# Performance work log

Measured on AMD Instinct MI355X. Metric: run time of the kernel, lower is better.

Reference implementation:

```python
import jax, jax.numpy as jnp
import numpy as np

B, T, C, H, W = 32, 64, 2, 32, 32
NK, KS = 16, 6          # n_kernels, kernel_size
ACT = 27                # conv output spatial size (32-6+1)
FEAT = ACT * ACT * NK   # 11664 flattened features
RU = 16                 # rnn_units
AD_RATE_L, REC_RATE_L = 0.1, 0.1   # AdaptiveLayer rates
AD_RATE_R, REC_RATE_R = 0.4, 0.1   # SimpleRNN rates


def setup_inputs() -> dict:
    key = jax.random.key(0)
    ks = jax.random.split(key, 8)
    stdv = 1.0 / np.sqrt(RU)
    return {
        "x": jax.random.normal(ks[0], (B, T, C, H, W), jnp.float32),
        "conv_w": jax.random.normal(ks[1], (NK, C, KS, KS), jnp.float32) * 0.01,
        "conv_b": jnp.full((NK,), 0.01, jnp.float32),
        "w_ih": jax.random.uniform(ks[2], (RU, FEAT), jnp.float32, -stdv, stdv),
        "w_hh": jax.random.uniform(ks[3], (RU, RU), jnp.float32, -stdv, stdv),
        "b_ih": jax.random.uniform(ks[4], (RU,), jnp.float32, -stdv, stdv),
        "b_hh": jax.random.uniform(ks[5], (RU,), jnp.float32, -stdv, stdv),
        "fc_w": jax.random.normal(ks[6], (2, RU), jnp.float32) * 0.01,
        "fc_b": jnp.full((2,), 0.01, jnp.float32),
    }


def reference(x, conv_w, conv_b, w_ih, w_hh, b_ih, b_hh, fc_w, fc_b):
    Bn, Tn = x.shape[:2]
    # per-frame conv: fold frames into batch
    xf = x.reshape(Bn * Tn, C, H, W)
    conv = jax.lax.conv_general_dilated(
        xf, conv_w, window_strides=(1, 1), padding='VALID',
        dimension_numbers=('NCHW', 'OIHW', 'NCHW'))
    conv = conv + conv_b[None, :, None, None]
    out_conv = conv.reshape(Bn, Tn, NK, ACT, ACT)
    out_flat = jax.nn.relu(out_conv.reshape(Bn, Tn, FEAT))

    # AdaptiveLayer: per-frame clamp/decay scan (initial adaptation is zeros)
    def ad_step(adapt, frame):
        out = jnp.maximum(frame - adapt, 0.0)
        adapt = (adapt + AD_RATE_L * out) * (1.0 - REC_RATE_L)
        return adapt, out
    _, adapted = jax.lax.scan(ad_step, jnp.zeros((Bn, FEAT), x.dtype),
                              jnp.swapaxes(out_flat, 0, 1))
    out_adapted = jnp.swapaxes(adapted, 0, 1)  # [B,T,FEAT]

    # SimpleRNN with adaptation state
    def rnn_step(carry, x_t):
        h, adapt = carry
        pre = x_t @ w_ih.T + b_ih + h @ w_hh.T + b_hh
        a = jnp.maximum(pre - adapt, 0.0)
        adapt = (adapt + AD_RATE_R * a) * (1.0 - REC_RATE_R)
        h = jax.nn.relu(a)
        return (h, adapt), h
    h0 = jnp.zeros((Bn, RU), x.dtype)
    _, hs = jax.lax.scan(rnn_step, (h0, h0), jnp.swapaxes(out_adapted, 0, 1))
    out_rnn = jnp.swapaxes(hs, 0, 1)  # [B,T,RU]

    out_fc = out_rnn @ fc_w.T + fc_b  # [B,T,2]
    return (out_fc, out_conv, out_flat, out_rnn)
```

## Files before the change

kernel.cpp:

```cpp
#include <hip/hip_runtime.h>

#define FEAT 11664
#define OFF_FC   0u
#define OFF_CONV 4096u
#define OFF_FLAT 23891968u
#define OFF_RNN  47779840u

static __device__ __forceinline__ unsigned short f2bf(float f) {
    unsigned int u = __float_as_uint(f);
    u += 0x7FFFu + ((u >> 16) & 1u);
    return (unsigned short)(u >> 16);
}

__global__ __launch_bounds__(128) void k_conv(const float* __restrict__ x,
                                              const float* __restrict__ cw,
                                              const float* __restrict__ cb,
                                              float* __restrict__ out)
{
    __shared__ __align__(16) float smem[11664];
    __shared__ float bls[16];
    float* xs  = smem;
    float* wls = smem + 2304;
    float* ot  = smem;
    const int tid = threadIdx.x;
    const int frame = blockIdx.x;

    const float4* xg = (const float4*)(x + (size_t)frame * 2048);
    for (int c0 = tid; c0 < 512; c0 += 128) {
        float4 v = xg[c0];
        int e0 = c0 * 4;
        int ch = e0 >> 10, rem = e0 & 1023, row = rem >> 5, col = rem & 31;
        float* dst = &xs[ch * 1152 + row * 36 + col];
        dst[0] = v.x; dst[1] = v.y; dst[2] = v.z; dst[3] = v.w;
    }
    for (int idx = tid; idx < 1152; idx += 128) {
        int k = idx / 72;
        int rem = idx - k * 72;
        wls[rem * 16 + k] = cw[idx];
    }
    if (tid < 16) bls[tid] = cb[tid];
    __syncthreads();

    const int kg = tid >> 5;
    const int r  = tid & 31;
    float acc[4][27];
    if (r < 27) {
        #pragma unroll
        for (int kk = 0; kk < 4; ++kk)
            #pragma unroll
            for (int c = 0; c < 27; ++c) acc[kk][c] = 0.f;

        for (int ch = 0; ch < 2; ++ch) {
            for (int i = 0; i < 6; ++i) {
                const float* rowp = &xs[ch * 1152 + (r + i) * 36];
                float xr[32];
                #pragma unroll
                for (int m = 0; m < 8; ++m) {
                    float4 v = ((const float4*)rowp)[m];
                    xr[4*m+0] = v.x; xr[4*m+1] = v.y; xr[4*m+2] = v.z; xr[4*m+3] = v.w;
                }
                float4 wj[6];
                #pragma unroll
                for (int j = 0; j < 6; ++j)
                    wj[j] = *(const float4*)&wls[(ch * 36 + i * 6 + j) * 16 + kg * 4];
                #pragma unroll
                for (int j = 0; j < 6; ++j) {
                    #pragma unroll
                    for (int c = 0; c < 27; ++c) {
                        float xv = xr[c + j];
                        acc[0][c] = fmaf(xv, wj[j].x, acc[0][c]);
                        acc[1][c] = fmaf(xv, wj[j].y, acc[1][c]);
                        acc[2][c] = fmaf(xv, wj[j].z, acc[2][c]);
                        acc[3][c] = fmaf(xv, wj[j].w, acc[3][c]);
                    }
                }
            }
        }
    }

    __syncthreads();
    if (r < 27) {
        #pragma unroll
        for (int kk = 0; kk < 4; ++kk) {
            float bv = bls[kg * 4 + kk];
            float* dst = &ot[(kg * 4 + kk) * 729 + r * 27];
            #pragma unroll
            for (int c = 0; c < 27; ++c) dst[c] = acc[kk][c] + bv;
        }
    }
    __syncthreads();

    const float4* src4 = (const float4*)ot;
    float4* dc = (float4*)(out + OFF_CONV + (size_t)frame * FEAT);
    float4* df = (float4*)(out + OFF_FLAT + (size_t)frame * FEAT);
    for (int e = tid; e < 2916; e += 128) {
        float4 v = src4[e];
        dc[e] = v;
        float4 rv;
        rv.x = v.x > 0.f ? v.x : 0.f;
        rv.y = v.y > 0.f ? v.y : 0.f;
        rv.z = v.z > 0.f ? v.z : 0.f;
        rv.w = v.w > 0.f ? v.w : 0.f;
        df[e] = rv;
    }
}

typedef short bf16x8 __attribute__((ext_vector_type(8)));
typedef float f32x4  __attribute__((ext_vector_type(4)));

__global__ __launch_bounds__(256) void k_adapt_proj(const float* __restrict__ flat,
                                                    const float* __restrict__ w_ih,
                                                    float* __restrict__ partial)
{
    __shared__ __align__(16) unsigned short A[16 * 744];
    __shared__ __align__(16) unsigned short Bw[16 * 744];
    __shared__ __align__(16) float accscr[4 * 64 * 4];
    const int tid = threadIdx.x;
    const int b  = blockIdx.x >> 4;
    const int fb = blockIdx.x & 15;
    const int fbase = fb * 729;

    float v0[16], v1[16], v2[16];
    const float* src0 = flat + (size_t)(b * 64) * FEAT + fbase + tid * 3;
    if (tid < 243) {
        #pragma unroll
        for (int tl = 0; tl < 16; ++tl) {
            const float* p = src0 + (size_t)tl * FEAT;
            v0[tl] = p[0]; v1[tl] = p[1]; v2[tl] = p[2];
        }
    }

    for (int n = 0; n < 16; ++n) {
        const float* src = w_ih + (size_t)n * FEAT + fbase;
        for (int f = tid; f < 729; f += 256) Bw[n * 744 + f] = f2bf(src[f]);
    }
    if (tid < 240) {
        int n = tid / 15, c = 729 + (tid % 15);
        A[n * 744 + c]  = 0;
        Bw[n * 744 + c] = 0;
    }
    __syncthreads();

    float ad0 = 0.f, ad1 = 0.f, ad2 = 0.f;
    const int w = tid >> 6, l = tid & 63;
    const int m = l & 15, q = l >> 4;

    for (int tt = 0; tt < 4; ++tt) {
        if (tid < 243) {
            unsigned short* arow = &A[tid * 3];
            #pragma unroll
            for (int tl = 0; tl < 16; ++tl) {
                float o0 = fmaxf(v0[tl] - ad0, 0.f); ad0 = (ad0 + 0.1f * o0) * 0.9f;
                float o1 = fmaxf(v1[tl] - ad1, 0.f); ad1 = (ad1 + 0.1f * o1) * 0.9f;
                float o2 = fmaxf(v2[tl] - ad2, 0.f); ad2 = (ad2 + 0.1f * o2) * 0.9f;
                unsigned short* dst = arow + tl * 744;
                dst[0] = f2bf(o0); dst[1] = f2bf(o1); dst[2] = f2bf(o2);
            }
        }
        __syncthreads();

        if (tt < 3 && tid < 243) {
            const float* srcn = flat + (size_t)(b * 64 + (tt + 1) * 16) * FEAT + fbase + tid * 3;
            #pragma unroll
            for (int tl = 0; tl < 16; ++tl) {
                const float* p = srcn + (size_t)tl * FEAT;
                v0[tl] = p[0]; v1[tl] = p[1]; v2[tl] = p[2];
            }
        }

        f32x4 acc = {0.f, 0.f, 0.f, 0.f};
        for (int s = w; s < 23; s += 4) {
            int k0 = s * 32;
            bf16x8 av = *(const bf16x8*)&A [m * 744 + k0 + q * 8];
            bf16x8 bv = *(const bf16x8*)&Bw[m * 744 + k0 + q * 8];
            acc = __builtin_amdgcn_mfma_f32_16x16x32_bf16(av, bv, acc, 0, 0, 0);
        }
        *(f32x4*)&accscr[(w * 64 + l) * 4] = acc;
        __syncthreads();
        {
            int ll = tid >> 2, rg = tid & 3;
            float s = accscr[(0 * 64 + ll) * 4 + rg] + accscr[(1 * 64 + ll) * 4 + rg]
                    + accscr[(2 * 64 + ll) * 4 + rg] + accscr[(3 * 64 + ll) * 4 + rg];
            int row = ((ll >> 4) * 4) + rg;
            int col = ll & 15;
            partial[(size_t)(((fb * 32 + b) * 64 + tt * 16 + row) * 16) + col] = s;
        }
        __syncthreads();
    }
}

__global__ __launch_bounds__(64) void k_rnn(const float* __restrict__ partial,
                                            const float* __restrict__ w_hh,
                                            const float* __restrict__ b_ih,
                                            const float* __restrict__ b_hh,
                                            const float* __restrict__ fc_w,
                                            const float* __restrict__ fc_b,
                                            float* __restrict__ out)
{
    __shared__ __align__(16) float preL[4096];
    __shared__ float hL[64];
    const int l = threadIdx.x;
    const int bl = l >> 4, u = l & 15;
    const int b = blockIdx.x * 4 + bl;

    const float4* p4 = (const float4*)partial;
    float4* pl4 = (float4*)preL;
    for (int c = l; c < 1024; c += 64) {
        float4 s = {0.f, 0.f, 0.f, 0.f};
        for (int fb = 0; fb < 16; ++fb) {
            float4 v = p4[(size_t)fb * 8192 + blockIdx.x * 1024 + c];
            s.x += v.x; s.y += v.y; s.z += v.z; s.w += v.w;
        }
        pl4[c] = s;
    }

    float wv[16];
    #pragma unroll
    for (int mm = 0; mm < 4; ++mm) {
        float4 t4 = *(const float4*)(w_hh + u * 16 + mm * 4);
        wv[4*mm+0] = t4.x; wv[4*mm+1] = t4.y; wv[4*mm+2] = t4.z; wv[4*mm+3] = t4.w;
    }
    const float bsum = b_ih[u] + b_hh[u];
    float frow[16]; float fcb = 0.f;
    if (u < 2) {
        #pragma unroll
        for (int mm = 0; mm < 4; ++mm) {
            float4 t4 = *(const float4*)(fc_w + u * 16 + mm * 4);
            frow[4*mm+0] = t4.x; frow[4*mm+1] = t4.y; frow[4*mm+2] = t4.z; frow[4*mm+3] = t4.w;
        }
        fcb = fc_b[u];
    }
    hL[l] = 0.f;
    float ad = 0.f;
    __syncthreads();

    for (int t = 0; t < 64; ++t) {
        float hv[16];
        #pragma unroll
        for (int mm = 0; mm < 4; ++mm) {
            float4 h4 = *(const float4*)&hL[bl * 16 + mm * 4];
            hv[4*mm+0] = h4.x; hv[4*mm+1] = h4.y; hv[4*mm+2] = h4.z; hv[4*mm+3] = h4.w;
        }
        if (t > 0 && u < 2) {
            float fcv = fcb;
            #pragma unroll
            for (int v2 = 0; v2 < 16; ++v2) fcv = fmaf(hv[v2], frow[v2], fcv);
            out[OFF_FC + (size_t)(b * 64 + (t - 1)) * 2 + u] = fcv;
        }
        float dot = 0.f;
        #pragma unroll
        for (int v2 = 0; v2 < 16; ++v2) dot = fmaf(hv[v2], wv[v2], dot);
        float v = preL[(bl * 64 + t) * 16 + u] + bsum + dot;
        float a = v - ad; a = a > 0.f ? a : 0.f;
        ad = (ad + 0.4f * a) * 0.9f;
        out[OFF_RNN + (size_t)(b * 64 + t) * 16 + u] = a;
        __syncthreads();
        hL[l] = a;
        __syncthreads();
    }
    {
        float hv[16];
        #pragma unroll
        for (int mm = 0; mm < 4; ++mm) {
            float4 h4 = *(const float4*)&hL[bl * 16 + mm * 4];
            hv[4*mm+0] = h4.x; hv[4*mm+1] = h4.y; hv[4*mm+2] = h4.z; hv[4*mm+3] = h4.w;
        }
        if (u < 2) {
            float fcv = fcb;
            #pragma unroll
            for (int v2 = 0; v2 < 16; ++v2) fcv = fmaf(hv[v2], frow[v2], fcv);
            out[OFF_FC + (size_t)(b * 64 + 63) * 2 + u] = fcv;
        }
    }
}

extern "C" void kernel_launch(void* const* d_in, const int* in_sizes, int n_in,
                              void* d_out, int out_size, void* d_ws, size_t ws_size,
                              hipStream_t stream)
{
    const float* x    = (const float*)d_in[0];
    const float* cw   = (const float*)d_in[1];
    const float* cb   = (const float*)d_in[2];
    const float* w_ih = (const float*)d_in[3];
    const float* w_hh = (const float*)d_in[4];
    const float* b_ih = (const float*)d_in[5];
    const float* b_hh = (const float*)d_in[6];
    const float* fc_w = (const float*)d_in[7];
    const float* fc_b = (const float*)d_in[8];
    float* out = (float*)d_out;
    float* partial = (float*)d_ws;

    k_conv<<<2048, 128, 0, stream>>>(x, cw, cb, out);
    k_adapt_proj<<<512, 256, 0, stream>>>(out + OFF_FLAT, w_ih, partial);
    k_rnn<<<8, 64, 0, stream>>>(partial, w_hh, b_ih, b_hh, fc_w, fc_b, out);
}
```

Before: 348.3 us.

## Split adaptation-projection over 48 feature chunks and drop single-wave RNN barriers

The adaptation plus input-projection kernel now splits the feature dimension into 48 chunks of 243 instead of 16 chunks of 729. This launches three times as many blocks with smaller shared-memory tiles, to use more of the GPU's compute units. In exchange, the RNN kernel must reduce three times as many partial sums, and that reduction runs in only 8 small blocks. The RNN kernel also drops its __syncthreads calls, since each block is a single 64-thread wavefront. The 48-chunk path is used only when the workspace is large enough; otherwise the old 16-chunk path runs.

```diff
diff --git a/kernel.cpp b/kernel.cpp
--- a/kernel.cpp
+++ b/kernel.cpp
@@ -108,9 +108,81 @@
 typedef short bf16x8 __attribute__((ext_vector_type(8)));
 typedef float f32x4  __attribute__((ext_vector_type(4)));
 
-__global__ __launch_bounds__(256) void k_adapt_proj(const float* __restrict__ flat,
-                                                    const float* __restrict__ w_ih,
-                                                    float* __restrict__ partial)
+__global__ __launch_bounds__(256) void k_adapt_proj48(const float* __restrict__ flat,
+                                                      const float* __restrict__ w_ih,
+                                                      float* __restrict__ partial)
+{
+    __shared__ __align__(16) unsigned short A[16 * 264];
+    __shared__ __align__(16) unsigned short Bw[16 * 264];
+    __shared__ __align__(16) float accscr[4 * 64 * 4];
+    const int tid = threadIdx.x;
+    const int b  = blockIdx.x / 48;
+    const int fb = blockIdx.x % 48;
+    const int fbase = fb * 243;
+
+    float v[16];
+    if (tid < 243) {
+        const float* p0 = flat + (size_t)(b * 64) * FEAT + fbase + tid;
+        #pragma unroll
+        for (int tl = 0; tl < 16; ++tl) v[tl] = p0[(size_t)tl * FEAT];
+    }
+
+    for (int n = 0; n < 16; ++n) {
+        if (tid < 243) Bw[n * 264 + tid] = f2bf(w_ih[(size_t)n * FEAT + fbase + tid]);
+    }
+    if (tid < 208) {
+        int n = tid / 13, c = 243 + tid % 13;
+        A[n * 264 + c]  = 0;
+        Bw[n * 264 + c] = 0;
+    }
+    __syncthreads();
+
+    float ad = 0.f;
+    const int w = tid >> 6, l = tid & 63;
+    const int m = l & 15, q = l >> 4;
+
+    for (int tt = 0; tt < 4; ++tt) {
+        if (tid < 243) {
+            unsigned short* arow = &A[tid];
+            #pragma unroll
+            for (int tl = 0; tl < 16; ++tl) {
+                float o = fmaxf(v[tl] - ad, 0.f); ad = (ad + 0.1f * o) * 0.9f;
+                arow[tl * 264] = f2bf(o);
+            }
+        }
+        __syncthreads();
+
+        if (tt < 3 && tid < 243) {
+            const float* pn = flat + (size_t)(b * 64 + (tt + 1) * 16) * FEAT + fbase + tid;
+            #pragma unroll
+            for (int tl = 0; tl < 16; ++tl) v[tl] = pn[(size_t)tl * FEAT];
+        }
+
+        f32x4 acc = {0.f, 0.f, 0.f, 0.f};
+        #pragma unroll
+        for (int s = w; s < 8; s += 4) {
+            int k0 = s * 32;
+            bf16x8 av = *(const bf16x8*)&A [m * 264 + k0 + q * 8];
+            bf16x8 bv = *(const bf16x8*)&Bw[m * 264 + k0 + q * 8];
+            acc = __builtin_amdgcn_mfma_f32_16x16x32_bf16(av, bv, acc, 0, 0, 0);
+        }
+        *(f32x4*)&accscr[(w * 64 + l) * 4] = acc;
+        __syncthreads();
+        {
+            int ll = tid >> 2, rg = tid & 3;
+            float s = accscr[(0 * 64 + ll) * 4 + rg] + accscr[(1 * 64 + ll) * 4 + rg]
+                    + accscr[(2 * 64 + ll) * 4 + rg] + accscr[(3 * 64 + ll) * 4 + rg];
+            int row = ((ll >> 4) * 4) + rg;
+            int col = ll & 15;
+            partial[(size_t)(((fb * 32 + b) * 64 + tt * 16 + row) * 16) + col] = s;
+        }
+        __syncthreads();
+    }
+}
+
+__global__ __launch_bounds__(256) void k_adapt_proj16(const float* __restrict__ flat,
+                                                      const float* __restrict__ w_ih,
+                                                      float* __restrict__ partial)
 {
     __shared__ __align__(16) unsigned short A[16 * 744];
     __shared__ __align__(16) unsigned short Bw[16 * 744];
@@ -189,13 +261,14 @@
     }
 }
 
-__global__ __launch_bounds__(64) void k_rnn(const float* __restrict__ partial,
-                                            const float* __restrict__ w_hh,
-                                            const float* __restrict__ b_ih,
-                                            const float* __restrict__ b_hh,
-                                            const float* __restrict__ fc_w,
-                                            const float* __restrict__ fc_b,
-                                            float* __restrict__ out)
+template<int NFB>
+__global__ __launch_bounds__(64) void k_rnn_t(const float* __restrict__ partial,
+                                              const float* __restrict__ w_hh,
+                                              const float* __restrict__ b_ih,
+                                              const float* __restrict__ b_hh,
+                                              const float* __restrict__ fc_w,
+                                              const float* __restrict__ fc_b,
+                                              float* __restrict__ out)
 {
     __shared__ __align__(16) float preL[4096];
     __shared__ float hL[64];
@@ -207,7 +280,7 @@
     float4* pl4 = (float4*)preL;
     for (int c = l; c < 1024; c += 64) {
         float4 s = {0.f, 0.f, 0.f, 0.f};
-        for (int fb = 0; fb < 16; ++fb) {
+        for (int fb = 0; fb < NFB; ++fb) {
             float4 v = p4[(size_t)fb * 8192 + blockIdx.x * 1024 + c];
             s.x += v.x; s.y += v.y; s.z += v.z; s.w += v.w;
         }
@@ -232,7 +305,6 @@
     }
     hL[l] = 0.f;
     float ad = 0.f;
-    __syncthreads();
 
     for (int t = 0; t < 64; ++t) {
         float hv[16];
@@ -254,9 +326,7 @@
         float a = v - ad; a = a > 0.f ? a : 0.f;
         ad = (ad + 0.4f * a) * 0.9f;
         out[OFF_RNN + (size_t)(b * 64 + t) * 16 + u] = a;
-        __syncthreads();
         hL[l] = a;
-        __syncthreads();
     }
     {
         float hv[16];
@@ -291,6 +361,13 @@
     float* partial = (float*)d_ws;
 
     k_conv<<<2048, 128, 0, stream>>>(x, cw, cb, out);
-    k_adapt_proj<<<512, 256, 0, stream>>>(out + OFF_FLAT, w_ih, partial);
-    k_rnn<<<8, 64, 0, stream>>>(partial, w_hh, b_ih, b_hh, fc_w, fc_b, out);
-}
+
+    const size_t need48 = 48ull * 32 * 64 * 16 * 4;
+    if (ws_size >= need48) {
+        k_adapt_proj48<<<1536, 256, 0, stream>>>(out + OFF_FLAT, w_ih, partial);
+        k_rnn_t<48><<<8, 64, 0, stream>>>(partial, w_hh, b_ih, b_hh, fc_w, fc_b, out);
+    } else {
+        k_adapt_proj16<<<512, 256, 0, stream>>>(out + OFF_FLAT, w_ih, partial);
+        k_rnn_t<16><<<8, 64, 0, stream>>>(partial, w_hh, b_ih, b_hh, fc_w, fc_b, out);
+    }
+}
```

New measurement: 316.2 us. 9.2% less time.
